# Kernel tuning notes

Hardware: AMD Instinct MI355X
Metric: run time of the kernel (lower is better)

The kernel has to match this reference:

```python
import jax, jax.numpy as jnp
import numpy as np

H = 4          # global_attention_heads
NL = 32        # num_landmark_tokens
STRIDE = 16    # landmark_stride
D = 3072       # hidden_size
HD = D // H    # head_dim = 768
SCALE = 1.0 / np.sqrt(HD).astype(np.float32)


def _landmark_indices(seq_len: int) -> jnp.ndarray:
    # torch: arange(0, seq_len, stride); if >NL, index with linspace(0, n-1, NL).long() (truncation)
    idx = np.arange(0, seq_len, STRIDE, dtype=np.int64)
    if len(idx) > NL:
        sel = np.linspace(0, len(idx) - 1, NL).astype(np.int64)  # truncates like torch long cast
        idx = idx[sel]
    return jnp.asarray(idx)


def _attn(q_in, kv_in, Wq, bq, Wk, bk, Wv, bv, Wo, bo):
    # shared QKV/O projections, standard multi-head attention q_in -> kv_in
    B, Lq, _ = q_in.shape
    Lk = kv_in.shape[1]
    Q = (q_in @ Wq + bq).reshape(B, Lq, H, HD)
    K = (kv_in @ Wk + bk).reshape(B, Lk, H, HD)
    V = (kv_in @ Wv + bv).reshape(B, Lk, H, HD)
    scores = jnp.einsum('bqhd,bkhd->bhqk', Q, K) * SCALE
    w = jax.nn.softmax(scores, axis=-1)  # dropout is identity in eval
    ctx = jnp.einsum('bhqk,bkhd->bqhd', w, V).reshape(B, Lq, D)
    return ctx @ Wo + bo


def setup_inputs() -> dict:
    key = jax.random.key(0)
    ks = jax.random.split(key, 10)
    B, S = 2, 8192
    s = 1.0 / np.sqrt(D).astype(np.float32)
    return {
        'hidden_states': jax.random.normal(ks[0], (B, S, D), jnp.float32),
        'landmark_emb': jax.random.normal(ks[1], (NL, D), jnp.float32),
        'Wq': jax.random.normal(ks[2], (D, D), jnp.float32) * s,
        'bq': jnp.zeros((D,), jnp.float32),
        'Wk': jax.random.normal(ks[3], (D, D), jnp.float32) * s,
        'bk': jnp.zeros((D,), jnp.float32),
        'Wv': jax.random.normal(ks[4], (D, D), jnp.float32) * s,
        'bv': jnp.zeros((D,), jnp.float32),
        'Wo': jax.random.normal(ks[5], (D, D), jnp.float32) * s,
        'bo': jnp.zeros((D,), jnp.float32),
    }


def reference(hidden_states, landmark_emb, Wq, bq, Wk, bk, Wv, bv, Wo, bo):
    B, S, _ = hidden_states.shape
    li = _landmark_indices(S)  # [NL], static
    # gather landmarks + learned landmark embeddings
    landmark_tokens = hidden_states[:, li, :] + landmark_emb[None]  # [B, NL, D]
    # all tokens attend to 32 landmarks
    global_out = _attn(hidden_states, landmark_tokens, Wq, bq, Wk, bk, Wv, bv, Wo, bo)  # [B,S,D]
    # landmarks attend to all tokens
    landmark_out = _attn(landmark_tokens, hidden_states, Wq, bq, Wk, bk, Wv, bv, Wo, bo)  # [B,NL,D]
    # scatter landmark outputs back (index_copy-style, replaces python loop)
    updated = hidden_states.at[:, li, :].set(landmark_out)
    return updated + global_out
```

## Files before the change

### kernel.cpp

```cpp
#include <hip/hip_runtime.h>
#include <stdint.h>

#define S_LEN   8192
#define DMODEL  3072
#define HDIM    768
#define NLM     32
#define MTOK    16384
#define MV      16448
#define MP      16512
#define NQKV    9216
#define KDIM    3072
#define NKT     48
#define SCALE_F 0.036084391824351615f

#define OFF_A    ((size_t)0)
#define OFF_WT   ((size_t)101449728)
#define OFF_QKV  ((size_t)176947200)
#define OFF_CTX  ((size_t)480116736)
#define OFF_BCAT ((size_t)581566464)
#define OFF_PART ((size_t)581615616)
#define OFF_KT   (OFF_PART)
#define OFF_VT   (OFF_PART + 393216)
#define OFF_ML2  (OFF_PART + 786432)
#define OFF_CP   (OFF_A)

#if defined(__has_builtin)
#if __has_builtin(__builtin_amdgcn_global_load_lds)
#define USE_GLL 1
#endif
#endif
#ifndef USE_GLL
#define USE_GLL 0
#endif

typedef __attribute__((ext_vector_type(8))) short bf8_t;
typedef __attribute__((ext_vector_type(4))) float f4_t;
typedef __attribute__((ext_vector_type(4))) short s4_t;
typedef __attribute__((ext_vector_type(4))) unsigned short us4_t;

__device__ __forceinline__ float b2f(unsigned short u) {
  unsigned x = ((unsigned)u) << 16;
  float f;
  __builtin_memcpy(&f, &x, 4);
  return f;
}
__device__ __forceinline__ unsigned short f2b(float f) {
  unsigned x;
  __builtin_memcpy(&x, &f, 4);
  x += 0x7fffu + ((x >> 16) & 1u);
  return (unsigned short)(x >> 16);
}
__device__ __forceinline__ void load12(const unsigned short* p, float* f) {
  s4_t v0 = *(const s4_t*)p;
  s4_t v1 = *(const s4_t*)(p + 4);
  s4_t v2 = *(const s4_t*)(p + 8);
#pragma unroll
  for (int e = 0; e < 4; ++e) {
    f[e]     = b2f((unsigned short)v0[e]);
    f[4 + e] = b2f((unsigned short)v1[e]);
    f[8 + e] = b2f((unsigned short)v2[e]);
  }
}
__device__ __forceinline__ void store12(unsigned short* p, const float* f) {
  us4_t a = {f2b(f[0]), f2b(f[1]), f2b(f[2]), f2b(f[3])};
  us4_t b = {f2b(f[4]), f2b(f[5]), f2b(f[6]), f2b(f[7])};
  us4_t c = {f2b(f[8]), f2b(f[9]), f2b(f[10]), f2b(f[11])};
  *(us4_t*)p = a;
  *(us4_t*)(p + 4) = b;
  *(us4_t*)(p + 8) = c;
}

__global__ __launch_bounds__(256) void build_bcat(const float* __restrict__ bq,
                                                  const float* __restrict__ bk,
                                                  const float* __restrict__ bv,
                                                  const float* __restrict__ bo,
                                                  float* __restrict__ bcat) {
  int n = blockIdx.x * 256 + threadIdx.x;
  float v = (n < 3072) ? bq[n] : (n < 6144) ? bk[n - 3072]
          : (n < 9216) ? bv[n - 6144] : bo[n - 9216];
  bcat[n] = v;
}

__global__ __launch_bounds__(256) void build_a(const float* __restrict__ hs,
                                               const float* __restrict__ lemb,
                                               unsigned short* __restrict__ A) {
  size_t idx = (size_t)blockIdx.x * 256 + threadIdx.x;
  size_t e = idx * 4;
  int row = (int)(e / DMODEL);
  int col = (int)(e - (size_t)row * DMODEL);
  f4_t v;
  if (row < MTOK) {
    v = *(const f4_t*)(hs + e);
  } else if (row < MV) {
    int r2 = row - MTOK;
    int b = r2 >> 5, j = r2 & 31;
    int sel = (j * 511) / 31;
    int li = sel * 16;
    f4_t a = *(const f4_t*)(hs + ((size_t)(b * S_LEN + li)) * DMODEL + col);
    f4_t c = *(const f4_t*)(lemb + (size_t)j * DMODEL + col);
    v = a + c;
  } else {
    v = (f4_t){0.f, 0.f, 0.f, 0.f};
  }
  us4_t o = {f2b(v[0]), f2b(v[1]), f2b(v[2]), f2b(v[3])};
  *(us4_t*)(A + e) = o;
}

__global__ __launch_bounds__(256) void wtrans(const float* __restrict__ W,
                                              unsigned short* __restrict__ Wt) {
  __shared__ float t[32][33];
  int n0 = blockIdx.x * 32, k0 = blockIdx.y * 32;
  int x = threadIdx.x, y = threadIdx.y;
#pragma unroll
  for (int i = 0; i < 4; ++i)
    t[y + i * 8][x] = W[(size_t)(k0 + y + i * 8) * DMODEL + n0 + x];
  __syncthreads();
#pragma unroll
  for (int i = 0; i < 4; ++i)
    Wt[(size_t)(n0 + y + i * 8) * DMODEL + k0 + x] = f2b(t[x][y + i * 8]);
}

#if USE_GLL
#define GLL16(SRC, OFF)                                                        \
  __builtin_amdgcn_global_load_lds(                                           \
      (const __attribute__((address_space(1))) void*)(SRC),                   \
      (__attribute__((address_space(3))) void*)(lds + (OFF)), 16, 0, 0)
#else
#define GLL16(SRC, OFF)                                                        \
  (*(bf8_t*)(lds + (OFF) + (unsigned)(threadIdx.x & 63) * 16) = *(const bf8_t*)(SRC))
#endif

#define STG_A(TT, KH, DD)                                                      \
  do {                                                                         \
    const unsigned short* _s = gA0 + (size_t)(TT) * 64 + (KH) * 32;            \
    GLL16(_s, (unsigned)((DD) * 32768 + (KH) * 16384) + wl16);                 \
    GLL16(_s + (size_t)128 * KDIM,                                             \
          (unsigned)((DD) * 32768 + (KH) * 16384 + 8192) + wl16);              \
  } while (0)
#define STG_B(TT, KH, DD)                                                      \
  do {                                                                         \
    const unsigned short* _s = gB0 + (size_t)(TT) * 64 + (KH) * 32;            \
    GLL16(_s, (unsigned)(65536 + (DD) * 32768 + (KH) * 16384) + wl16);         \
    GLL16(_s + (size_t)128 * KDIM,                                             \
          (unsigned)(65536 + (DD) * 32768 + (KH) * 16384 + 8192) + wl16);      \
  } while (0)

#define LDA8(DD, KH, QM, MI)                                                   \
  (*(const bf8_t*)(lds + (DD) * 32768 + (KH) * 16384 + aBase + (QM) * 4096 +   \
                   (MI) * 1024))
#define LDB8(DD, KH, NI)                                                       \
  (*(const bf8_t*)(lds + (DD) * 32768 + (KH) * 16384 + bBase + (NI) * 1024))

#define MFMA16(Q, A0, A1, A2, A3, B0, B1, B2, B3)                              \
  do {                                                                         \
    __builtin_amdgcn_s_setprio(1);                                             \
    acc[(Q)+0][0] = __builtin_amdgcn_mfma_f32_16x16x32_bf16(A0, B0, acc[(Q)+0][0], 0, 0, 0); \
    acc[(Q)+1][0] = __builtin_amdgcn_mfma_f32_16x16x32_bf16(A1, B0, acc[(Q)+1][0], 0, 0, 0); \
    acc[(Q)+2][0] = __builtin_amdgcn_mfma_f32_16x16x32_bf16(A2, B0, acc[(Q)+2][0], 0, 0, 0); \
    acc[(Q)+3][0] = __builtin_amdgcn_mfma_f32_16x16x32_bf16(A3, B0, acc[(Q)+3][0], 0, 0, 0); \
    acc[(Q)+0][1] = __builtin_amdgcn_mfma_f32_16x16x32_bf16(A0, B1, acc[(Q)+0][1], 0, 0, 0); \
    acc[(Q)+1][1] = __builtin_amdgcn_mfma_f32_16x16x32_bf16(A1, B1, acc[(Q)+1][1], 0, 0, 0); \
    acc[(Q)+2][1] = __builtin_amdgcn_mfma_f32_16x16x32_bf16(A2, B1, acc[(Q)+2][1], 0, 0, 0); \
    acc[(Q)+3][1] = __builtin_amdgcn_mfma_f32_16x16x32_bf16(A3, B1, acc[(Q)+3][1], 0, 0, 0); \
    acc[(Q)+0][2] = __builtin_amdgcn_mfma_f32_16x16x32_bf16(A0, B2, acc[(Q)+0][2], 0, 0, 0); \
    acc[(Q)+1][2] = __builtin_amdgcn_mfma_f32_16x16x32_bf16(A1, B2, acc[(Q)+1][2], 0, 0, 0); \
    acc[(Q)+2][2] = __builtin_amdgcn_mfma_f32_16x16x32_bf16(A2, B2, acc[(Q)+2][2], 0, 0, 0); \
    acc[(Q)+3][2] = __builtin_amdgcn_mfma_f32_16x16x32_bf16(A3, B2, acc[(Q)+3][2], 0, 0, 0); \
    acc[(Q)+0][3] = __builtin_amdgcn_mfma_f32_16x16x32_bf16(A0, B3, acc[(Q)+0][3], 0, 0, 0); \
    acc[(Q)+1][3] = __builtin_amdgcn_mfma_f32_16x16x32_bf16(A1, B3, acc[(Q)+1][3], 0, 0, 0); \
    acc[(Q)+2][3] = __builtin_amdgcn_mfma_f32_16x16x32_bf16(A2, B3, acc[(Q)+2][3], 0, 0, 0); \
    acc[(Q)+3][3] = __builtin_amdgcn_mfma_f32_16x16x32_bf16(A3, B3, acc[(Q)+3][3], 0, 0, 0); \
    __builtin_amdgcn_s_setprio(0);                                             \
  } while (0)

__global__ __launch_bounds__(512, 2) void gemm256(const unsigned short* __restrict__ A,
                                                  const unsigned short* __restrict__ Bt,
                                                  const float* __restrict__ bias,
                                                  unsigned short* __restrict__ C,
                                                  int Mvalid, int N, int Ntiles) {
  extern __shared__ char lds[];
  const int tid = threadIdx.x;
  const int lane = tid & 63;
  const int wave = tid >> 6;
  const int WM = wave >> 2;
  const int WN = wave & 3;
  const int row16 = lane & 15, quad = lane >> 4;

  int nwg = (int)gridDim.x;
  int orig = (int)blockIdx.x;
  int q = nwg >> 3, r = nwg & 7;
  int xcd = orig & 7, lin = orig >> 3;
  int wg = (xcd < r ? xcd * (q + 1) : r * (q + 1) + (xcd - r) * q) + lin;
  const int tileM = (wg / Ntiles) * 256;
  const int tileN = (wg % Ntiles) * 256;

  const int srow2 = tid >> 2;
  const int scq = (tid & 3) ^ ((srow2 >> 1) & 3);
  const unsigned short* gA0 = A + (size_t)(tileM + srow2) * KDIM + scq * 8;
  const unsigned short* gB0 = Bt + (size_t)(tileN + srow2) * KDIM + scq * 8;
  const unsigned wl16 = (unsigned)(tid & 448) * 16;

  const unsigned co = (unsigned)((quad * 16) ^ (((row16 >> 1) & 3) << 4));
  const unsigned aBase = (unsigned)(WM * 8192 + row16 * 64) + co;
  const unsigned bBase = 65536u + (unsigned)(WN * 4096 + row16 * 64) + co;

  f4_t acc[8][4];
#pragma unroll
  for (int a = 0; a < 8; ++a)
#pragma unroll
    for (int b = 0; b < 4; ++b) acc[a][b] = (f4_t){0.f, 0.f, 0.f, 0.f};

  STG_B(0, 0, 0); STG_A(0, 0, 0); STG_B(0, 1, 0); STG_A(0, 1, 0);
  STG_B(1, 0, 1); STG_A(1, 0, 1); STG_B(1, 1, 1);
  asm volatile("s_waitcnt vmcnt(6)" ::: "memory");
  __builtin_amdgcn_s_barrier();

#pragma unroll 2
  for (int t = 0; t < NKT; ++t) {
    const int d = t & 1;
    bf8_t a00 = LDA8(d, 0, 0, 0), a01 = LDA8(d, 0, 0, 1),
          a02 = LDA8(d, 0, 0, 2), a03 = LDA8(d, 0, 0, 3);
    bf8_t b00 = LDB8(d, 0, 0), b01 = LDB8(d, 0, 1),
          b02 = LDB8(d, 0, 2), b03 = LDB8(d, 0, 3);
    {
      if (t + 1 < NKT) STG_A(t + 1, 1, d ^ 1);
      bf8_t a10 = LDA8(d, 0, 1, 0), a11 = LDA8(d, 0, 1, 1),
            a12 = LDA8(d, 0, 1, 2), a13 = LDA8(d, 0, 1, 3);
      __builtin_amdgcn_s_barrier();
      MFMA16(0, a00, a01, a02, a03, b00, b01, b02, b03);
      __builtin_amdgcn_s_barrier();
      if (t + 2 < NKT) STG_B(t + 2, 0, d);
      bf8_t a20 = LDA8(d, 1, 0, 0), a21 = LDA8(d, 1, 0, 1),
            a22 = LDA8(d, 1, 0, 2), a23 = LDA8(d, 1, 0, 3);
      bf8_t b10 = LDB8(d, 1, 0), b11 = LDB8(d, 1, 1),
            b12 = LDB8(d, 1, 2), b13 = LDB8(d, 1, 3);
      __builtin_amdgcn_s_barrier();
      MFMA16(4, a10, a11, a12, a13, b00, b01, b02, b03);
      __builtin_amdgcn_s_barrier();
      if (t + 2 < NKT) STG_A(t + 2, 0, d);
      bf8_t a30 = LDA8(d, 1, 1, 0), a31 = LDA8(d, 1, 1, 1),
            a32 = LDA8(d, 1, 1, 2), a33 = LDA8(d, 1, 1, 3);
      __builtin_amdgcn_s_barrier();
      MFMA16(0, a20, a21, a22, a23, b10, b11, b12, b13);
      __builtin_amdgcn_s_barrier();
      if (t + 2 < NKT) STG_B(t + 2, 1, d);
      __builtin_amdgcn_s_barrier();
      MFMA16(4, a30, a31, a32, a33, b10, b11, b12, b13);
      if (t + 2 < NKT) asm volatile("s_waitcnt vmcnt(6)" ::: "memory");
      else             asm volatile("s_waitcnt vmcnt(0)" ::: "memory");
      __builtin_amdgcn_s_barrier();
    }
  }

  float bv_[4];
#pragma unroll
  for (int ni = 0; ni < 4; ++ni) bv_[ni] = bias[tileN + WN * 64 + ni * 16 + row16];
#pragma unroll
  for (int mi = 0; mi < 8; ++mi) {
#pragma unroll
    for (int i = 0; i < 4; ++i) {
      int grow = tileM + WM * 128 + mi * 16 + quad * 4 + i;
      if (grow < Mvalid) {
        size_t base = (size_t)grow * N + tileN + WN * 64 + row16;
#pragma unroll
        for (int ni = 0; ni < 4; ++ni)
          C[base + ni * 16] = f2b(acc[mi][ni][i] + bv_[ni]);
      }
    }
  }
}

__global__ __launch_bounds__(256) void kv_prep(const unsigned short* __restrict__ QKV,
                                               unsigned short* __restrict__ KT,
                                               unsigned short* __restrict__ VT) {
  int idx = blockIdx.x * 256 + threadIdx.x;
  if (idx < 24576) {
    int bh = idx / 3072, i = idx % 3072;
    int b = bh >> 2, h = bh & 3;
    int j = i & 31, c = i >> 5;
    bf8_t v = *(const bf8_t*)(QKV + (size_t)(MTOK + b * NLM + j) * NQKV + DMODEL +
                              h * HDIM + c * 8);
    *(bf8_t*)(KT + (size_t)bh * 24576 + (size_t)(c * 32 + j) * 8) = v;
  } else {
    int i2 = idx - 24576;
    int bh = i2 / 3072, r = i2 % 3072;
    int b = bh >> 2, h = bh & 3;
    int d = r >> 2, slot = r & 3;
    unsigned short vals[8];
#pragma unroll
    for (int e = 0; e < 8; ++e)
      vals[e] = QKV[(size_t)(MTOK + b * NLM + slot * 8 + e) * NQKV + 2 * DMODEL +
                    h * HDIM + d];
    unsigned short* p = VT + (size_t)bh * 24576 + (size_t)d * 32 + slot * 8;
    *(us4_t*)p = (us4_t){vals[0], vals[1], vals[2], vals[3]};
    *(us4_t*)(p + 4) = (us4_t){vals[4], vals[5], vals[6], vals[7]};
  }
}

__global__ __launch_bounds__(256, 2) void glob_attn(const unsigned short* __restrict__ QKV,
                                                    const unsigned short* __restrict__ KT,
                                                    const unsigned short* __restrict__ VT,
                                                    unsigned short* __restrict__ CTX) {
  __shared__ unsigned short P_s[4][32][32];
  const int tid = threadIdx.x;
  const int lane = tid & 63;
  const int w = tid >> 6;
  const int row16 = lane & 15, quad = lane >> 4;

  const int qt = blockIdx.x & 63;
  const int h = (blockIdx.x >> 6) & 3;
  const int b = blockIdx.x >> 8;
  const int bh = b * 4 + h;
  const int rowbase = b * S_LEN + qt * 128 + w * 32;

  const unsigned short* KTb = KT + (size_t)bh * 24576;
  const unsigned short* VTb = VT + (size_t)bh * 24576;

  f4_t sc[2][2];
#pragma unroll
  for (int mi = 0; mi < 2; ++mi)
#pragma unroll
    for (int ni = 0; ni < 2; ++ni) sc[mi][ni] = (f4_t){0.f, 0.f, 0.f, 0.f};

#pragma unroll
  for (int kt = 0; kt < 24; ++kt) {
    bf8_t kb0 = *(const bf8_t*)(KTb + (size_t)((kt * 4 + quad) * 32 + row16) * 8);
    bf8_t kb1 = *(const bf8_t*)(KTb + (size_t)((kt * 4 + quad) * 32 + 16 + row16) * 8);
    bf8_t qa0 = *(const bf8_t*)(QKV + (size_t)(rowbase + row16) * NQKV + h * HDIM +
                                kt * 32 + quad * 8);
    bf8_t qa1 = *(const bf8_t*)(QKV + (size_t)(rowbase + 16 + row16) * NQKV + h * HDIM +
                                kt * 32 + quad * 8);
    sc[0][0] = __builtin_amdgcn_mfma_f32_16x16x32_bf16(qa0, kb0, sc[0][0], 0, 0, 0);
    sc[0][1] = __builtin_amdgcn_mfma_f32_16x16x32_bf16(qa0, kb1, sc[0][1], 0, 0, 0);
    sc[1][0] = __builtin_amdgcn_mfma_f32_16x16x32_bf16(qa1, kb0, sc[1][0], 0, 0, 0);
    sc[1][1] = __builtin_amdgcn_mfma_f32_16x16x32_bf16(qa1, kb1, sc[1][1], 0, 0, 0);
  }

#pragma unroll
  for (int mi = 0; mi < 2; ++mi) {
#pragma unroll
    for (int i = 0; i < 4; ++i) {
      float s0 = sc[mi][0][i] * SCALE_F;
      float s1 = sc[mi][1][i] * SCALE_F;
      float mx = fmaxf(s0, s1);
#pragma unroll
      for (int off = 8; off; off >>= 1) mx = fmaxf(mx, __shfl_xor(mx, off));
      float p0 = __expf(s0 - mx), p1 = __expf(s1 - mx);
      float sum = p0 + p1;
#pragma unroll
      for (int off = 8; off; off >>= 1) sum += __shfl_xor(sum, off);
      float inv = 1.f / sum;
      int rr = mi * 16 + quad * 4 + i;
      P_s[w][rr][row16] = f2b(p0 * inv);
      P_s[w][rr][16 + row16] = f2b(p1 * inv);
    }
  }
  __syncthreads();

  bf8_t pa0 = *(const bf8_t*)&P_s[w][row16][quad * 8];
  bf8_t pa1 = *(const bf8_t*)&P_s[w][16 + row16][quad * 8];
  unsigned short* ctxb = CTX + (size_t)rowbase * DMODEL + h * HDIM;

#pragma unroll
  for (int dch = 0; dch < 12; ++dch) {
    bf8_t vb[4];
#pragma unroll
    for (int ni = 0; ni < 4; ++ni)
      vb[ni] = *(const bf8_t*)(VTb + (size_t)(dch * 64 + ni * 16 + row16) * 32 + quad * 8);
#pragma unroll
    for (int mi = 0; mi < 2; ++mi) {
      bf8_t pa = mi ? pa1 : pa0;
#pragma unroll
      for (int ni = 0; ni < 4; ++ni) {
        f4_t c = __builtin_amdgcn_mfma_f32_16x16x32_bf16(
            pa, vb[ni], (f4_t){0.f, 0.f, 0.f, 0.f}, 0, 0, 0);
#pragma unroll
        for (int i = 0; i < 4; ++i)
          ctxb[(size_t)(mi * 16 + quad * 4 + i) * DMODEL + dch * 64 + ni * 16 + row16] =
              f2b(c[i]);
      }
    }
  }
}

__global__ __launch_bounds__(256, 2) void lm_attn_part(const unsigned short* __restrict__ QKV,
                                                       float* __restrict__ ctxpart,
                                                       float* __restrict__ mlpart) {
  int wid = blockIdx.x * 4 + (threadIdx.x >> 6);
  int lane = threadIdx.x & 63;
  int jg = wid & 3, kc = (wid >> 2) & 63, h = (wid >> 8) & 3, b = wid >> 10;

  float qreg[8][12];
#pragma unroll
  for (int jj = 0; jj < 8; ++jj)
    load12(QKV + (size_t)(MTOK + b * NLM + jg * 8 + jj) * NQKV + h * HDIM + lane * 12,
           qreg[jj]);

  float m[8], l[8], ctx[8][12];
#pragma unroll
  for (int jj = 0; jj < 8; ++jj) {
    m[jj] = -1e30f;
    l[jj] = 0.f;
#pragma unroll
    for (int e = 0; e < 12; ++e) ctx[jj][e] = 0.f;
  }

  for (int k = kc * 128; k < kc * 128 + 128; ++k) {
    size_t row = (size_t)(b * S_LEN + k);
    float kv[12], vv[12];
    load12(QKV + row * NQKV + DMODEL + h * HDIM + lane * 12, kv);
    float s[8];
#pragma unroll
    for (int jj = 0; jj < 8; ++jj) {
      float p = 0.f;
#pragma unroll
      for (int e = 0; e < 12; ++e) p += qreg[jj][e] * kv[e];
      s[jj] = p;
    }
#pragma unroll
    for (int jj = 0; jj < 8; ++jj) {
#pragma unroll
      for (int off = 32; off; off >>= 1) s[jj] += __shfl_xor(s[jj], off);
      s[jj] *= SCALE_F;
    }
    load12(QKV + row * NQKV + 2 * DMODEL + h * HDIM + lane * 12, vv);
#pragma unroll
    for (int jj = 0; jj < 8; ++jj) {
      if (s[jj] <= m[jj]) {
        float pp = __expf(s[jj] - m[jj]);
        l[jj] += pp;
#pragma unroll
        for (int e = 0; e < 12; ++e) ctx[jj][e] += pp * vv[e];
      } else {
        float al = __expf(m[jj] - s[jj]);
        m[jj] = s[jj];
        l[jj] = l[jj] * al + 1.f;
#pragma unroll
        for (int e = 0; e < 12; ++e) ctx[jj][e] = ctx[jj][e] * al + vv[e];
      }
    }
  }

#pragma unroll
  for (int jj = 0; jj < 8; ++jj) {
    int p = (((b * 4 + h) * 32) + (jg * 8 + jj)) * 64 + kc;
    float* cp = ctxpart + (size_t)p * HDIM + lane * 12;
#pragma unroll
    for (int e = 0; e < 12; ++e) cp[e] = ctx[jj][e];
    if (lane == 0) {
      mlpart[p * 2] = m[jj];
      mlpart[p * 2 + 1] = l[jj];
    }
  }
}

__global__ __launch_bounds__(256) void lm_combine(const float* __restrict__ ctxpart,
                                                  const float* __restrict__ mlpart,
                                                  unsigned short* __restrict__ CTX) {
  int wid = blockIdx.x * 4 + (threadIdx.x >> 6);
  int lane = threadIdx.x & 63;
  int j = wid & 31, h = (wid >> 5) & 3, b = wid >> 7;
  int base = wid * 64;
  float mk = mlpart[(base + lane) * 2];
  float lk = mlpart[(base + lane) * 2 + 1];
  float mm = mk;
#pragma unroll
  for (int off = 32; off; off >>= 1) mm = fmaxf(mm, __shfl_xor(mm, off));
  float al = __expf(mk - mm);
  float ls = al * lk;
#pragma unroll
  for (int off = 32; off; off >>= 1) ls += __shfl_xor(ls, off);

  float ctx[12];
#pragma unroll
  for (int e = 0; e < 12; ++e) ctx[e] = 0.f;
  for (int kc = 0; kc < 64; ++kc) {
    float a = __shfl(al, kc);
    const float* cp = ctxpart + (size_t)(base + kc) * HDIM + lane * 12;
#pragma unroll
    for (int e = 0; e < 12; ++e) ctx[e] += a * cp[e];
  }
  float inv = 1.f / ls;
#pragma unroll
  for (int e = 0; e < 12; ++e) ctx[e] *= inv;
  store12(CTX + (size_t)(MTOK + b * NLM + j) * DMODEL + h * HDIM + lane * 12, ctx);
}

__global__ __launch_bounds__(256) void compose(const float* __restrict__ hs,
                                               const unsigned short* __restrict__ PROJ,
                                               float* __restrict__ out) {
  size_t idx = (size_t)blockIdx.x * 256 + threadIdx.x;
  size_t e = idx * 4;
  int row = (int)(e / DMODEL);
  int col = (int)(e - (size_t)row * DMODEL);
  int b = row >> 13, s = row & (S_LEN - 1);

  us4_t g4 = *(const us4_t*)(PROJ + (size_t)row * DMODEL + col);
  int j = -1;
  if ((s & 15) == 0) {
    int sel = s >> 4;
    int jc = (sel * 31 + 510) / 511;
    if (jc < 32 && (jc * 511) / 31 == sel) j = jc;
  }
  f4_t base;
  if (j >= 0) {
    us4_t l4 = *(const us4_t*)(PROJ + (size_t)(MTOK + b * NLM + j) * DMODEL + col);
    base = (f4_t){b2f(l4[0]), b2f(l4[1]), b2f(l4[2]), b2f(l4[3])};
  } else {
    base = *(const f4_t*)(hs + e);
  }
  f4_t o = {base[0] + b2f(g4[0]), base[1] + b2f(g4[1]),
            base[2] + b2f(g4[2]), base[3] + b2f(g4[3])};
  *(f4_t*)(out + e) = o;
}

extern "C" void kernel_launch(void* const* d_in, const int* in_sizes, int n_in,
                              void* d_out, int out_size, void* d_ws, size_t ws_size,
                              hipStream_t stream) {
  const float* hs   = (const float*)d_in[0];
  const float* lemb = (const float*)d_in[1];
  const float* Wq   = (const float*)d_in[2];
  const float* bq   = (const float*)d_in[3];
  const float* Wk   = (const float*)d_in[4];
  const float* bk   = (const float*)d_in[5];
  const float* Wv   = (const float*)d_in[6];
  const float* bv   = (const float*)d_in[7];
  const float* Wo   = (const float*)d_in[8];
  const float* bo   = (const float*)d_in[9];
  float* out = (float*)d_out;
  char* ws = (char*)d_ws;

  unsigned short* A    = (unsigned short*)(ws + OFF_A);
  unsigned short* Wt   = (unsigned short*)(ws + OFF_WT);
  unsigned short* QKV  = (unsigned short*)(ws + OFF_QKV);
  unsigned short* CTX  = (unsigned short*)(ws + OFF_CTX);
  float*          bcat = (float*)(ws + OFF_BCAT);
  unsigned short* KT   = (unsigned short*)(ws + OFF_KT);
  unsigned short* VT   = (unsigned short*)(ws + OFF_VT);
  float*          ml   = (float*)(ws + OFF_ML2);
  float*          cpart= (float*)(ws + OFF_CP);
  unsigned short* PROJ = (unsigned short*)(ws + OFF_A);

  static bool attr_set = false;
  if (!attr_set) {
    (void)hipFuncSetAttribute(reinterpret_cast<const void*>(gemm256),
                              hipFuncAttributeMaxDynamicSharedMemorySize, 131072);
    attr_set = true;
  }

  build_bcat<<<dim3(48), dim3(256), 0, stream>>>(bq, bk, bv, bo, bcat);
  build_a<<<dim3(49536), dim3(256), 0, stream>>>(hs, lemb, A);
  wtrans<<<dim3(96, 96), dim3(32, 8), 0, stream>>>(Wq, Wt);
  wtrans<<<dim3(96, 96), dim3(32, 8), 0, stream>>>(Wk, Wt + (size_t)3072 * KDIM);
  wtrans<<<dim3(96, 96), dim3(32, 8), 0, stream>>>(Wv, Wt + (size_t)6144 * KDIM);
  wtrans<<<dim3(96, 96), dim3(32, 8), 0, stream>>>(Wo, Wt + (size_t)9216 * KDIM);

  gemm256<<<dim3(65 * 36), dim3(512), 131072, stream>>>(A, Wt, bcat, QKV, MV, NQKV, 36);

  kv_prep<<<dim3(192), dim3(256), 0, stream>>>(QKV, KT, VT);
  glob_attn<<<dim3(512), dim3(256), 0, stream>>>(QKV, KT, VT, CTX);
  lm_attn_part<<<dim3(512), dim3(256), 0, stream>>>(QKV, cpart, ml);
  lm_combine<<<dim3(64), dim3(256), 0, stream>>>(cpart, ml, CTX);

  gemm256<<<dim3(65 * 12), dim3(512), 131072, stream>>>(
      CTX, Wt + (size_t)9216 * KDIM, bcat + 9216, PROJ, MV, DMODEL, 12);

  compose<<<dim3(49152), dim3(256), 0, stream>>>(hs, PROJ, out);
}
```

Before: 2.114 ms.

## Group GEMM tiles by N-bands, restructure LDS/MFMA schedule, merge weight transposes

The GEMM's workgroup-to-tile mapping now walks groups of 8 N-tiles across all M-tiles, so that concurrently running workgroups share B-operand columns in cache. The main loop also loads fewer LDS fragments ahead of each MFMA block and adds explicit lgkmcnt waits, which lowers register pressure but may expose more LDS latency. The four weight-transpose launches are merged into a single launch using blockIdx.z.

```diff
diff --git a/kernel.cpp b/kernel.cpp
--- a/kernel.cpp
+++ b/kernel.cpp
@@ -11,6 +11,7 @@
 #define NQKV    9216
 #define KDIM    3072
 #define NKT     48
+#define MTILES  65
 #define SCALE_F 0.036084391824351615f
 
 #define OFF_A    ((size_t)0)
@@ -106,9 +107,15 @@
   *(us4_t*)(A + e) = o;
 }
 
-__global__ __launch_bounds__(256) void wtrans(const float* __restrict__ W,
-                                              unsigned short* __restrict__ Wt) {
+__global__ __launch_bounds__(256) void wtrans4(const float* __restrict__ W0,
+                                               const float* __restrict__ W1,
+                                               const float* __restrict__ W2,
+                                               const float* __restrict__ W3,
+                                               unsigned short* __restrict__ Wt) {
   __shared__ float t[32][33];
+  const float* Wsel[4] = {W0, W1, W2, W3};
+  const float* W = Wsel[blockIdx.z];
+  unsigned short* dst = Wt + (size_t)blockIdx.z * 3072 * KDIM;
   int n0 = blockIdx.x * 32, k0 = blockIdx.y * 32;
   int x = threadIdx.x, y = threadIdx.y;
 #pragma unroll
@@ -117,7 +124,7 @@
   __syncthreads();
 #pragma unroll
   for (int i = 0; i < 4; ++i)
-    Wt[(size_t)(n0 + y + i * 8) * DMODEL + k0 + x] = f2b(t[x][y + i * 8]);
+    dst[(size_t)(n0 + y + i * 8) * DMODEL + k0 + x] = f2b(t[x][y + i * 8]);
 }
 
 #if USE_GLL
@@ -191,8 +198,15 @@
   int q = nwg >> 3, r = nwg & 7;
   int xcd = orig & 7, lin = orig >> 3;
   int wg = (xcd < r ? xcd * (q + 1) : r * (q + 1) + (xcd - r) * q) + lin;
-  const int tileM = (wg / Ntiles) * 256;
-  const int tileN = (wg % Ntiles) * 256;
+
+  int g = wg / (MTILES * 8);
+  int w2 = wg - g * (MTILES * 8);
+  int Ng = Ntiles - g * 8;
+  int m_, nl;
+  if (Ng >= 8) { m_ = w2 >> 3; nl = w2 & 7; }
+  else         { m_ = w2 / Ng; nl = w2 - m_ * Ng; }
+  const int tileM = m_ * 256;
+  const int tileN = (g * 8 + nl) * 256;
 
   const int srow2 = tid >> 2;
   const int scq = (tid & 3) ^ ((srow2 >> 1) & 3);
@@ -218,34 +232,40 @@
 #pragma unroll 2
   for (int t = 0; t < NKT; ++t) {
     const int d = t & 1;
-    bf8_t a00 = LDA8(d, 0, 0, 0), a01 = LDA8(d, 0, 0, 1),
-          a02 = LDA8(d, 0, 0, 2), a03 = LDA8(d, 0, 0, 3);
-    bf8_t b00 = LDB8(d, 0, 0), b01 = LDB8(d, 0, 1),
-          b02 = LDB8(d, 0, 2), b03 = LDB8(d, 0, 3);
     {
+      bf8_t a0 = LDA8(d, 0, 0, 0), a1 = LDA8(d, 0, 0, 1),
+            a2 = LDA8(d, 0, 0, 2), a3 = LDA8(d, 0, 0, 3);
+      bf8_t b0 = LDB8(d, 0, 0), b1 = LDB8(d, 0, 1),
+            b2 = LDB8(d, 0, 2), b3 = LDB8(d, 0, 3);
       if (t + 1 < NKT) STG_A(t + 1, 1, d ^ 1);
-      bf8_t a10 = LDA8(d, 0, 1, 0), a11 = LDA8(d, 0, 1, 1),
-            a12 = LDA8(d, 0, 1, 2), a13 = LDA8(d, 0, 1, 3);
-      __builtin_amdgcn_s_barrier();
-      MFMA16(0, a00, a01, a02, a03, b00, b01, b02, b03);
-      __builtin_amdgcn_s_barrier();
+      __builtin_amdgcn_s_barrier();
+      asm volatile("s_waitcnt lgkmcnt(0)");
+      MFMA16(0, a0, a1, a2, a3, b0, b1, b2, b3);
+      __builtin_amdgcn_s_barrier();
+      bf8_t a4 = LDA8(d, 0, 1, 0), a5 = LDA8(d, 0, 1, 1),
+            a6 = LDA8(d, 0, 1, 2), a7 = LDA8(d, 0, 1, 3);
       if (t + 2 < NKT) STG_B(t + 2, 0, d);
-      bf8_t a20 = LDA8(d, 1, 0, 0), a21 = LDA8(d, 1, 0, 1),
-            a22 = LDA8(d, 1, 0, 2), a23 = LDA8(d, 1, 0, 3);
-      bf8_t b10 = LDB8(d, 1, 0), b11 = LDB8(d, 1, 1),
-            b12 = LDB8(d, 1, 2), b13 = LDB8(d, 1, 3);
-      __builtin_amdgcn_s_barrier();
-      MFMA16(4, a10, a11, a12, a13, b00, b01, b02, b03);
-      __builtin_amdgcn_s_barrier();
+      __builtin_amdgcn_s_barrier();
+      asm volatile("s_waitcnt lgkmcnt(0)");
+      MFMA16(4, a4, a5, a6, a7, b0, b1, b2, b3);
+      __builtin_amdgcn_s_barrier();
+    }
+    {
+      bf8_t a0 = LDA8(d, 1, 0, 0), a1 = LDA8(d, 1, 0, 1),
+            a2 = LDA8(d, 1, 0, 2), a3 = LDA8(d, 1, 0, 3);
+      bf8_t b0 = LDB8(d, 1, 0), b1 = LDB8(d, 1, 1),
+            b2 = LDB8(d, 1, 2), b3 = LDB8(d, 1, 3);
       if (t + 2 < NKT) STG_A(t + 2, 0, d);
-      bf8_t a30 = LDA8(d, 1, 1, 0), a31 = LDA8(d, 1, 1, 1),
-            a32 = LDA8(d, 1, 1, 2), a33 = LDA8(d, 1, 1, 3);
-      __builtin_amdgcn_s_barrier();
-      MFMA16(0, a20, a21, a22, a23, b10, b11, b12, b13);
-      __builtin_amdgcn_s_barrier();
+      __builtin_amdgcn_s_barrier();
+      asm volatile("s_waitcnt lgkmcnt(0)");
+      MFMA16(0, a0, a1, a2, a3, b0, b1, b2, b3);
+      __builtin_amdgcn_s_barrier();
+      bf8_t a4 = LDA8(d, 1, 1, 0), a5 = LDA8(d, 1, 1, 1),
+            a6 = LDA8(d, 1, 1, 2), a7 = LDA8(d, 1, 1, 3);
       if (t + 2 < NKT) STG_B(t + 2, 1, d);
       __builtin_amdgcn_s_barrier();
-      MFMA16(4, a30, a31, a32, a33, b10, b11, b12, b13);
+      asm volatile("s_waitcnt lgkmcnt(0)");
+      MFMA16(4, a4, a5, a6, a7, b0, b1, b2, b3);
       if (t + 2 < NKT) asm volatile("s_waitcnt vmcnt(6)" ::: "memory");
       else             asm volatile("s_waitcnt vmcnt(0)" ::: "memory");
       __builtin_amdgcn_s_barrier();
@@ -550,10 +570,7 @@
 
   build_bcat<<<dim3(48), dim3(256), 0, stream>>>(bq, bk, bv, bo, bcat);
   build_a<<<dim3(49536), dim3(256), 0, stream>>>(hs, lemb, A);
-  wtrans<<<dim3(96, 96), dim3(32, 8), 0, stream>>>(Wq, Wt);
-  wtrans<<<dim3(96, 96), dim3(32, 8), 0, stream>>>(Wk, Wt + (size_t)3072 * KDIM);
-  wtrans<<<dim3(96, 96), dim3(32, 8), 0, stream>>>(Wv, Wt + (size_t)6144 * KDIM);
-  wtrans<<<dim3(96, 96), dim3(32, 8), 0, stream>>>(Wo, Wt + (size_t)9216 * KDIM);
+  wtrans4<<<dim3(96, 96, 4), dim3(32, 8), 0, stream>>>(Wq, Wk, Wv, Wo, Wt);
 
   gemm256<<<dim3(65 * 36), dim3(512), 131072, stream>>>(A, Wt, bcat, QKV, MV, NQKV, 36);
 
```

Measured after the change: 2.048 ms. 1.03x faster.
